# Kernel tuning notes

Hardware: AMD Instinct MI355X
Metric: run time of the kernel (lower is better)

## Reference

```python
import jax, jax.numpy as jnp
import numpy as np

N = 65536   # base nodes
M = 65536   # union local nodes
E = 1048576 # base edges
EL = 1048576 # local edges
K = 131072  # membership entries
F = 128     # in_channels
H = 128     # hidden_dim
L = 2       # num_layers
OUT = 2
ALPHA = 0.9


def setup_inputs() -> dict:
    key = jax.random.key(0)
    ks = jax.random.split(key, 16)
    s = 1.0 / np.sqrt(H)
    return {
        "x": jax.random.normal(ks[0], (N, F), jnp.float32),
        "edge_index": jax.random.randint(ks[1], (2, E), 0, N, jnp.int64 if jax.config.jax_enable_x64 else jnp.int32),
        "edge_weight": jax.random.uniform(ks[2], (E,), jnp.float32),
        "local_x0": jax.random.normal(ks[3], (M, F), jnp.float32),
        "copy2orig": jax.random.randint(ks[4], (M,), 0, N),
        "local_adj_index": jax.random.randint(ks[5], (2, EL), 0, M),
        "local_adj_value": jax.random.uniform(ks[6], (EL,), jnp.float32),
        "memb_idx": jax.random.randint(ks[7], (K,), 0, M),
        "memb_gid": jax.random.randint(ks[8], (K,), 0, 64),
        "B": 64,
        "Wb_in": jax.random.normal(ks[9], (F, H), jnp.float32) * s,
        "bb_in": jnp.zeros((H,), jnp.float32),
        "Wl_in": jax.random.normal(ks[10], (F, H), jnp.float32) * s,
        "bl_in": jnp.zeros((H,), jnp.float32),
        "W_base": jax.random.normal(ks[11], (L, H, H), jnp.float32) * s,
        "b_base": jnp.zeros((L, H), jnp.float32),
        "W_local": jax.random.normal(ks[12], (L, H, H), jnp.float32) * s,
        "b_local": jnp.zeros((L, H), jnp.float32),
        "Wp": jax.random.normal(ks[13], (H, OUT), jnp.float32) * s,
        "bp": jnp.zeros((OUT,), jnp.float32),
    }


def reference(x, edge_index, edge_weight, local_x0, copy2orig, local_adj_index,
              local_adj_value, memb_idx, memb_gid, B, Wb_in, bb_in, Wl_in, bl_in,
              W_base, b_base, W_local, b_local, Wp, bp):
    n = x.shape[0]
    m = local_x0.shape[0]
    # input projections (dropout is identity in eval mode)
    base_x = jax.nn.relu(x @ Wb_in + bb_in)
    local_x = jax.nn.relu(local_x0 @ Wl_in + bl_in)
    src, dst = edge_index[0], edge_index[1]
    lsrc, ldst = local_adj_index[0], local_adj_index[1]
    for l in range(W_base.shape[0]):
        # base graph propagation: normalized-adjacency spmm then linear+relu
        base_agg = jax.ops.segment_sum(base_x[src] * edge_weight[:, None], dst, num_segments=n)
        base_x = jax.nn.relu(base_agg @ W_base[l] + b_base[l])
        # local union-graph propagation + alpha-mix with base features via copy2orig
        local_agg = jax.ops.segment_sum(local_x[lsrc] * local_adj_value[:, None], ldst, num_segments=m)
        mix = ALPHA * local_agg + (1.0 - ALPHA) * base_x[copy2orig]
        local_x = jax.nn.relu(mix @ W_local[l] + b_local[l])
    # scatter-mean pooling by membership (fused sum + count)
    sub = jax.ops.segment_sum(local_x[memb_idx], memb_gid, num_segments=B)
    cnt = jax.ops.segment_sum(jnp.ones((memb_gid.shape[0], 1), local_x.dtype), memb_gid, num_segments=B)
    sub = sub / jnp.maximum(cnt, 1.0)
    return sub @ Wp + bp
```

## Files before the change

kernel.cpp:

```cpp
#include <hip/hip_runtime.h>

typedef __attribute__((ext_vector_type(8))) short bfrag;
typedef __attribute__((ext_vector_type(4))) float ffrag;

__device__ __forceinline__ ushort f2bf(float f) {
    union { float f; unsigned u; } v{f};
    unsigned r = v.u + 0x7fff + ((v.u >> 16) & 1);
    return (ushort)(r >> 16);
}
__device__ __forceinline__ float bf2f(ushort u) {
    union { unsigned u; float f; } v{(unsigned)u << 16};
    return v.f;
}
__device__ __forceinline__ float bflo(unsigned u) {
    union { unsigned u; float f; } v{u << 16};
    return v.f;
}
__device__ __forceinline__ float bfhi(unsigned u) {
    union { unsigned u; float f; } v{u & 0xffff0000u};
    return v.f;
}

#define WDEC (1.f / 65535.f)


__global__ __launch_bounds__(256) void wprep_zero(const float* __restrict__ Wb_in, const float* __restrict__ Wl_in,
                                                  const float* __restrict__ W_base, const float* __restrict__ W_local,
                                                  ushort* __restrict__ out,
                                                  int* __restrict__ z_a, int* __restrict__ z_b,
                                                  int* __restrict__ z_c, int* __restrict__ z_d) {
    const int bid = blockIdx.x;
    const int t = threadIdx.x;
    if (bid < 384) {
        int idx = bid * 256 + t;
        int mat = idx >> 14;
        int i = idx & 16383;
        int nn = i >> 7, kk = i & 127;
        const float* src;
        switch (mat) {
            case 0: src = Wb_in; break;
            case 1: src = Wl_in; break;
            case 2: src = W_base; break;
            case 3: src = W_base + 16384; break;
            case 4: src = W_local; break;
            default: src = W_local + 16384; break;
        }
        out[(size_t)mat * 16384 + i] = f2bf(src[kk * 128 + nn]);
    } else {
        int i = (bid - 384) * 256 + t;
        if (i < 512) { z_a[i] = 0; z_b[i] = 0; }
        if (i < 64) z_c[i] = 0;
        z_d[i] = 0;
    }
}


#define NB 512
#define BSH 7
#define CH2 2048

__global__ __launch_bounds__(256) void hist2p(const int* __restrict__ b_dst, const int* __restrict__ l_dst,
                                              int* __restrict__ b_cnt, int* __restrict__ l_cnt,
                                              const int* __restrict__ memb_gid, int* __restrict__ gcount) {
    __shared__ int h[NB];
    const int bid = blockIdx.x;
    const int t = threadIdx.x;
    if (bid < 512) {
        h[t] = 0;
        h[t + 256] = 0;
        __syncthreads();
        const int g = bid >> 8;
        const int* dst = g ? l_dst : b_dst;
        int* cnt = g ? l_cnt : b_cnt;
        const int base = (bid & 255) * 4096;
#pragma unroll
        for (int u = 0; u < 16; ++u)
            atomicAdd(&h[((unsigned)dst[base + u * 256 + t]) >> BSH], 1);
        __syncthreads();
        atomicAdd(&cnt[t], h[t]);
        atomicAdd(&cnt[t + 256], h[t + 256]);
    } else {
        if (t < 64) h[t] = 0;
        __syncthreads();
        const int base = (bid - 512) * 1024;
#pragma unroll
        for (int u = 0; u < 4; ++u) atomicAdd(&h[memb_gid[base + u * 256 + t]], 1);
        __syncthreads();
        if (t < 64) atomicAdd(&gcount[t], h[t]);
    }
}

__global__ __launch_bounds__(512) void scan2p(const int* __restrict__ b_cnt, int* __restrict__ b_sta, int* __restrict__ b_cur,
                                              const int* __restrict__ l_cnt, int* __restrict__ l_sta, int* __restrict__ l_cur,
                                              const int* __restrict__ gcount, int* __restrict__ gstart,
                                              int* __restrict__ cursor) {
    __shared__ int s[NB];
    const int t = threadIdx.x;
    if (blockIdx.x < 2) {
        const int* cnt = blockIdx.x ? l_cnt : b_cnt;
        int* sta = blockIdx.x ? l_sta : b_sta;
        int* cur = blockIdx.x ? l_cur : b_cur;
        int c = cnt[t];
        s[t] = c;
        __syncthreads();
        for (int o = 1; o < NB; o <<= 1) {
            int add = (t >= o) ? s[t - o] : 0;
            __syncthreads();
            s[t] += add;
            __syncthreads();
        }
        sta[t] = s[t] - c;
        cur[t] = s[t] - c;
        if (t == NB - 1) sta[NB] = s[t];
    } else {
        int c = 0;
        if (t < 64) { c = gcount[t]; s[t] = c; }
        __syncthreads();
        if (t < 64) {
            int acc = 0;
            for (int j = 0; j < t; ++j) acc += s[j];
            gstart[t] = acc;
            cursor[t] = acc;
            if (t == 63) gstart[64] = acc + c;
        }
    }
}

__global__ __launch_bounds__(512) void bucket1b(const int* __restrict__ b_src, const int* __restrict__ b_dst,
                                                const float* __restrict__ b_w, int* __restrict__ b_cur,
                                                int2* __restrict__ b_staged,
                                                const int* __restrict__ l_src, const int* __restrict__ l_dst,
                                                const float* __restrict__ l_w, int* __restrict__ l_cur,
                                                int2* __restrict__ l_staged) {
    __shared__ int cnt_s[NB], base_l[NB], base_g[NB], curs[NB];
    __shared__ int2 stage[CH2];
    __shared__ ushort bb[CH2];
    const int t = threadIdx.x;
    const int g = blockIdx.x >> 9;
    const int* src = g ? l_src : b_src;
    const int* dst = g ? l_dst : b_dst;
    const float* w = g ? l_w : b_w;
    int* bcursor = g ? l_cur : b_cur;
    int2* staged = g ? l_staged : b_staged;
    const int base = (blockIdx.x & 511) * CH2;
    cnt_s[t] = 0;
    __syncthreads();
#pragma unroll
    for (int u = 0; u < CH2 / 512; ++u) {
        int b = ((unsigned)dst[base + u * 512 + t]) >> BSH;
        atomicAdd(&cnt_s[b], 1);
    }
    __syncthreads();
    int v = cnt_s[t];
    base_l[t] = v;
    __syncthreads();
    for (int o = 1; o < NB; o <<= 1) {
        int add = (t >= o) ? base_l[t - o] : 0;
        __syncthreads();
        base_l[t] += add;
        __syncthreads();
    }
    {
        int excl = base_l[t] - v;
        base_l[t] = excl;
        curs[t] = excl;
        base_g[t] = atomicAdd(&bcursor[t], v);
    }
    __syncthreads();
#pragma unroll
    for (int u = 0; u < CH2 / 512; ++u) {
        int e = base + u * 512 + t;
        int d = dst[e];
        int b = ((unsigned)d) >> BSH;
        int p = atomicAdd(&curs[b], 1);
        stage[p] = make_int2((src[e] & 0xffff) | ((d & 127) << 16), __float_as_int(w[e]));
        bb[p] = (ushort)b;
    }
    __syncthreads();
    for (int i = t; i < CH2; i += 512) {
        int b = bb[i];
        staged[base_g[b] + (i - base_l[b])] = stage[i];
    }
}

__global__ __launch_bounds__(512) void bucket2b(const int* __restrict__ b_sta, const int2* __restrict__ b_staged,
                                                int* __restrict__ b_start, int* __restrict__ b_edges,
                                                const int* __restrict__ l_sta, const int2* __restrict__ l_staged,
                                                int* __restrict__ l_start, int* __restrict__ l_edges) {
    __shared__ int cnt[128], excl[128], curs[128];
    const int t = threadIdx.x;
    const int g = blockIdx.x >> 9;
    const int b = blockIdx.x & 511;
    const int* bsta = g ? l_sta : b_sta;
    const int2* staged = g ? l_staged : b_staged;
    int* start = g ? l_start : b_start;
    int* edges = g ? l_edges : b_edges;
    if (t < 128) cnt[t] = 0;
    __syncthreads();
    const int s0 = bsta[b];
    const int s1 = bsta[b + 1];
    for (int i = s0 + t; i < s1; i += 512) {
        int dl = (staged[i].x >> 16) & 127;
        atomicAdd(&cnt[dl], 1);
    }
    __syncthreads();
    int v = 0;
    if (t < 128) { v = cnt[t]; excl[t] = v; }
    __syncthreads();
    for (int o = 1; o < 128; o <<= 1) {
        int add = 0;
        if (t < 128 && t >= o) add = excl[t - o];
        __syncthreads();
        if (t < 128) excl[t] += add;
        __syncthreads();
    }
    if (t < 128) {
        int e = excl[t] - v;
        curs[t] = e;
        start[b * 128 + t] = s0 + e;
        if (b == 511 && t == 127) start[65536] = s1;
    }
    __syncthreads();
    for (int i = s0 + t; i < s1; i += 512) {
        int2 se = staged[i];
        int dl = (se.x >> 16) & 127;
        int p = s0 + atomicAdd(&curs[dl], 1);
        float wv = __int_as_float(se.y);
        unsigned wq = (unsigned)(wv * 65535.f + 0.5f);
        edges[p] = (int)(((unsigned)se.x & 0xffffu) | (wq << 16));
    }
}

#define ASTRIDE 136


__global__ __launch_bounds__(256) void gemm_in2(const float* __restrict__ Ab, const float* __restrict__ Al,
                                                const ushort* __restrict__ Wt,
                                                const float* __restrict__ biasb, const float* __restrict__ biasl,
                                                ushort* __restrict__ Yb, ushort* __restrict__ Yl) {
    __shared__ ushort As[64 * ASTRIDE];
    __shared__ ushort Bs[128 * ASTRIDE];
    const int tid = threadIdx.x;
    const int g = blockIdx.x >> 10;
    const float* A = g ? Al : Ab;
    const ushort* W = Wt + (size_t)g * 16384;
    const float* bias = g ? biasl : biasb;
    ushort* Y = g ? Yl : Yb;
    const int r0 = (blockIdx.x & 1023) * 64;

#pragma unroll
    for (int p = 0; p < 8; ++p) {
        int c = p * 256 + tid;
        int row = c >> 5, o4 = (c & 31) * 4;
        float4 v = *(const float4*)(A + (size_t)(r0 + row) * 128 + o4);
        ushort4 u;
        u.x = f2bf(v.x); u.y = f2bf(v.y); u.z = f2bf(v.z); u.w = f2bf(v.w);
        *(ushort4*)&As[row * ASTRIDE + o4] = u;
    }
#pragma unroll
    for (int p = 0; p < 8; ++p) {
        int c = p * 256 + tid;
        int n = c >> 4, o8 = (c & 15) * 8;
        *(uint4*)&Bs[n * ASTRIDE + o8] = *(const uint4*)(W + n * 128 + o8);
    }
    __syncthreads();

    const int lane = tid & 63;
    const int w = tid >> 6;
    const int wm = (w & 1) * 32;
    const int wn = (w >> 1) * 64;
    const int q = lane >> 4;
    const int l16 = lane & 15;

    ffrag acc[2][4];
#pragma unroll
    for (int mt = 0; mt < 2; ++mt)
#pragma unroll
        for (int nt = 0; nt < 4; ++nt) acc[mt][nt] = (ffrag){0.f, 0.f, 0.f, 0.f};

#pragma unroll
    for (int kc = 0; kc < 4; ++kc) {
        bfrag a[2], b[4];
#pragma unroll
        for (int mt = 0; mt < 2; ++mt)
            a[mt] = *(const bfrag*)&As[(wm + mt * 16 + l16) * ASTRIDE + kc * 32 + q * 8];
#pragma unroll
        for (int nt = 0; nt < 4; ++nt)
            b[nt] = *(const bfrag*)&Bs[(wn + nt * 16 + l16) * ASTRIDE + kc * 32 + q * 8];
#pragma unroll
        for (int mt = 0; mt < 2; ++mt)
#pragma unroll
            for (int nt = 0; nt < 4; ++nt)
                acc[mt][nt] = __builtin_amdgcn_mfma_f32_16x16x32_bf16(a[mt], b[nt], acc[mt][nt], 0, 0, 0);
    }

    float bias_v[4];
#pragma unroll
    for (int nt = 0; nt < 4; ++nt) bias_v[nt] = bias[wn + nt * 16 + l16];
#pragma unroll
    for (int mt = 0; mt < 2; ++mt)
#pragma unroll
        for (int nt = 0; nt < 4; ++nt)
#pragma unroll
            for (int r = 0; r < 4; ++r) {
                int row = r0 + wm + mt * 16 + q * 4 + r;
                int col = wn + nt * 16 + l16;
                float v = fmaxf(acc[mt][nt][r] + bias_v[nt], 0.f);
                Y[(size_t)row * 128 + col] = f2bf(v);
            }
}


template <bool MIX>
__global__ __launch_bounds__(256) void gemm_layer(const ushort* __restrict__ A, const ushort* __restrict__ A2,
                                                  const int* __restrict__ ridx,
                                                  const ushort* __restrict__ Wt, const float* __restrict__ bias,
                                                  ushort* __restrict__ Y) {
    __shared__ ushort As[64 * ASTRIDE];
    __shared__ ushort Bs[128 * ASTRIDE];
    const int tid = threadIdx.x;
    const int r0 = blockIdx.x * 64;

#pragma unroll
    for (int p = 0; p < 4; ++p) {
        int c = p * 256 + tid;
        int row = c >> 4, o8 = (c & 15) * 8;
        uint4 v = *(const uint4*)(A + (size_t)(r0 + row) * 128 + o8);
        if (MIX) {
            int rr = ridx[r0 + row];
            uint4 v2 = *(const uint4*)(A2 + (size_t)rr * 128 + o8);
            uint4 o;
            float x0, x1;
            x0 = 0.9f * bflo(v.x) + 0.1f * bflo(v2.x);
            x1 = 0.9f * bfhi(v.x) + 0.1f * bfhi(v2.x);
            o.x = (unsigned)f2bf(x0) | ((unsigned)f2bf(x1) << 16);
            x0 = 0.9f * bflo(v.y) + 0.1f * bflo(v2.y);
            x1 = 0.9f * bfhi(v.y) + 0.1f * bfhi(v2.y);
            o.y = (unsigned)f2bf(x0) | ((unsigned)f2bf(x1) << 16);
            x0 = 0.9f * bflo(v.z) + 0.1f * bflo(v2.z);
            x1 = 0.9f * bfhi(v.z) + 0.1f * bfhi(v2.z);
            o.z = (unsigned)f2bf(x0) | ((unsigned)f2bf(x1) << 16);
            x0 = 0.9f * bflo(v.w) + 0.1f * bflo(v2.w);
            x1 = 0.9f * bfhi(v.w) + 0.1f * bfhi(v2.w);
            o.w = (unsigned)f2bf(x0) | ((unsigned)f2bf(x1) << 16);
            v = o;
        }
        *(uint4*)&As[row * ASTRIDE + o8] = v;
    }
#pragma unroll
    for (int p = 0; p < 8; ++p) {
        int c = p * 256 + tid;
        int n = c >> 4, o8 = (c & 15) * 8;
        *(uint4*)&Bs[n * ASTRIDE + o8] = *(const uint4*)(Wt + n * 128 + o8);
    }
    __syncthreads();

    const int lane = tid & 63;
    const int w = tid >> 6;
    const int wm = (w & 1) * 32;
    const int wn = (w >> 1) * 64;
    const int q = lane >> 4;
    const int l16 = lane & 15;

    ffrag acc[2][4];
#pragma unroll
    for (int mt = 0; mt < 2; ++mt)
#pragma unroll
        for (int nt = 0; nt < 4; ++nt) acc[mt][nt] = (ffrag){0.f, 0.f, 0.f, 0.f};

#pragma unroll
    for (int kc = 0; kc < 4; ++kc) {
        bfrag a[2], b[4];
#pragma unroll
        for (int mt = 0; mt < 2; ++mt)
            a[mt] = *(const bfrag*)&As[(wm + mt * 16 + l16) * ASTRIDE + kc * 32 + q * 8];
#pragma unroll
        for (int nt = 0; nt < 4; ++nt)
            b[nt] = *(const bfrag*)&Bs[(wn + nt * 16 + l16) * ASTRIDE + kc * 32 + q * 8];
#pragma unroll
        for (int mt = 0; mt < 2; ++mt)
#pragma unroll
            for (int nt = 0; nt < 4; ++nt)
                acc[mt][nt] = __builtin_amdgcn_mfma_f32_16x16x32_bf16(a[mt], b[nt], acc[mt][nt], 0, 0, 0);
    }

    float bias_v[4];
#pragma unroll
    for (int nt = 0; nt < 4; ++nt) bias_v[nt] = bias[wn + nt * 16 + l16];
#pragma unroll
    for (int mt = 0; mt < 2; ++mt)
#pragma unroll
        for (int nt = 0; nt < 4; ++nt)
#pragma unroll
            for (int r = 0; r < 4; ++r) {
                int row = r0 + wm + mt * 16 + q * 4 + r;
                int col = wn + nt * 16 + l16;
                float v = fmaxf(acc[mt][nt][r] + bias_v[nt], 0.f);
                Y[(size_t)row * 128 + col] = f2bf(v);
            }
}


__global__ __launch_bounds__(256) void spmm2(const int* __restrict__ bs_start, const int* __restrict__ bs_edges,
                                             const ushort* __restrict__ Xb, ushort* __restrict__ Yb,
                                             const int* __restrict__ ls_start, const int* __restrict__ ls_edges,
                                             const ushort* __restrict__ Xl, ushort* __restrict__ Yl) {
    const int g = blockIdx.x & 1;
    const int* start = g ? ls_start : bs_start;
    const int* edges = g ? ls_edges : bs_edges;
    const ushort* X = g ? Xl : Xb;
    ushort* Y = g ? Yl : Yb;
    int node = (((blockIdx.x >> 1) * 256) + threadIdx.x) >> 5;
    int lane = threadIdx.x & 31;
    int s0 = start[node];
    int s1 = start[node + 1];
    const int f = lane * 4;
    float a0 = 0.f, a1 = 0.f, a2 = 0.f, a3 = 0.f;
    int e = s0;
    for (; e < s1 && (e & 3); ++e) {
        unsigned pe = (unsigned)edges[e];
        float w = (float)(pe >> 16) * WDEC;
        ushort4 v = *(const ushort4*)(X + ((size_t)(pe & 0xffffu) << 7) + f);
        a0 += w * bf2f(v.x); a1 += w * bf2f(v.y); a2 += w * bf2f(v.z); a3 += w * bf2f(v.w);
    }
    for (; e + 8 <= s1; e += 8) {
        int4 pA = *(const int4*)(edges + e);
        int4 pB = *(const int4*)(edges + e + 4);
        ushort4 v0 = *(const ushort4*)(X + ((size_t)((unsigned)pA.x & 0xffffu) << 7) + f);
        ushort4 v1 = *(const ushort4*)(X + ((size_t)((unsigned)pA.y & 0xffffu) << 7) + f);
        ushort4 v2 = *(const ushort4*)(X + ((size_t)((unsigned)pA.z & 0xffffu) << 7) + f);
        ushort4 v3 = *(const ushort4*)(X + ((size_t)((unsigned)pA.w & 0xffffu) << 7) + f);
        ushort4 v4 = *(const ushort4*)(X + ((size_t)((unsigned)pB.x & 0xffffu) << 7) + f);
        ushort4 v5 = *(const ushort4*)(X + ((size_t)((unsigned)pB.y & 0xffffu) << 7) + f);
        ushort4 v6 = *(const ushort4*)(X + ((size_t)((unsigned)pB.z & 0xffffu) << 7) + f);
        ushort4 v7 = *(const ushort4*)(X + ((size_t)((unsigned)pB.w & 0xffffu) << 7) + f);
        float w0 = (float)((unsigned)pA.x >> 16) * WDEC;
        float w1 = (float)((unsigned)pA.y >> 16) * WDEC;
        float w2 = (float)((unsigned)pA.z >> 16) * WDEC;
        float w3 = (float)((unsigned)pA.w >> 16) * WDEC;
        float w4 = (float)((unsigned)pB.x >> 16) * WDEC;
        float w5 = (float)((unsigned)pB.y >> 16) * WDEC;
        float w6 = (float)((unsigned)pB.z >> 16) * WDEC;
        float w7 = (float)((unsigned)pB.w >> 16) * WDEC;
        a0 += w0 * bf2f(v0.x) + w1 * bf2f(v1.x) + w2 * bf2f(v2.x) + w3 * bf2f(v3.x)
            + w4 * bf2f(v4.x) + w5 * bf2f(v5.x) + w6 * bf2f(v6.x) + w7 * bf2f(v7.x);
        a1 += w0 * bf2f(v0.y) + w1 * bf2f(v1.y) + w2 * bf2f(v2.y) + w3 * bf2f(v3.y)
            + w4 * bf2f(v4.y) + w5 * bf2f(v5.y) + w6 * bf2f(v6.y) + w7 * bf2f(v7.y);
        a2 += w0 * bf2f(v0.z) + w1 * bf2f(v1.z) + w2 * bf2f(v2.z) + w3 * bf2f(v3.z)
            + w4 * bf2f(v4.z) + w5 * bf2f(v5.z) + w6 * bf2f(v6.z) + w7 * bf2f(v7.z);
        a3 += w0 * bf2f(v0.w) + w1 * bf2f(v1.w) + w2 * bf2f(v2.w) + w3 * bf2f(v3.w)
            + w4 * bf2f(v4.w) + w5 * bf2f(v5.w) + w6 * bf2f(v6.w) + w7 * bf2f(v7.w);
    }
    for (; e + 4 <= s1; e += 4) {
        int4 pA = *(const int4*)(edges + e);
        ushort4 v0 = *(const ushort4*)(X + ((size_t)((unsigned)pA.x & 0xffffu) << 7) + f);
        ushort4 v1 = *(const ushort4*)(X + ((size_t)((unsigned)pA.y & 0xffffu) << 7) + f);
        ushort4 v2 = *(const ushort4*)(X + ((size_t)((unsigned)pA.z & 0xffffu) << 7) + f);
        ushort4 v3 = *(const ushort4*)(X + ((size_t)((unsigned)pA.w & 0xffffu) << 7) + f);
        float w0 = (float)((unsigned)pA.x >> 16) * WDEC;
        float w1 = (float)((unsigned)pA.y >> 16) * WDEC;
        float w2 = (float)((unsigned)pA.z >> 16) * WDEC;
        float w3 = (float)((unsigned)pA.w >> 16) * WDEC;
        a0 += w0 * bf2f(v0.x) + w1 * bf2f(v1.x) + w2 * bf2f(v2.x) + w3 * bf2f(v3.x);
        a1 += w0 * bf2f(v0.y) + w1 * bf2f(v1.y) + w2 * bf2f(v2.y) + w3 * bf2f(v3.y);
        a2 += w0 * bf2f(v0.z) + w1 * bf2f(v1.z) + w2 * bf2f(v2.z) + w3 * bf2f(v3.z);
        a3 += w0 * bf2f(v0.w) + w1 * bf2f(v1.w) + w2 * bf2f(v2.w) + w3 * bf2f(v3.w);
    }
    for (; e < s1; ++e) {
        unsigned pe = (unsigned)edges[e];
        float w = (float)(pe >> 16) * WDEC;
        ushort4 v = *(const ushort4*)(X + ((size_t)(pe & 0xffffu) << 7) + f);
        a0 += w * bf2f(v.x); a1 += w * bf2f(v.y); a2 += w * bf2f(v.z); a3 += w * bf2f(v.w);
    }
    ushort4 o;
    o.x = f2bf(a0);
    o.y = f2bf(a1);
    o.z = f2bf(a2);
    o.w = f2bf(a3);
    *(ushort4*)(Y + (size_t)node * 128 + f) = o;
}


__global__ __launch_bounds__(256) void pool_scatter(const int* __restrict__ memb_idx,
                                                    const int* __restrict__ memb_gid,
                                                    int* __restrict__ cursor, int* __restrict__ sorted_idx) {
    __shared__ int lhist[64];
    __shared__ int lbase[64];
    __shared__ int loff[1024];
    int t = threadIdx.x;
    if (t < 64) lhist[t] = 0;
    __syncthreads();
    int base = blockIdx.x * 1024;
    int g[4], ix[4];
#pragma unroll
    for (int u = 0; u < 4; ++u) {
        int e = base + u * 256 + t;
        g[u] = memb_gid[e];
        ix[u] = memb_idx[e];
        loff[u * 256 + t] = atomicAdd(&lhist[g[u]], 1);
    }
    __syncthreads();
    if (t < 64) lbase[t] = atomicAdd(&cursor[t], lhist[t]);
    __syncthreads();
#pragma unroll
    for (int u = 0; u < 4; ++u) {
        int pos = lbase[g[u]] + loff[u * 256 + t];
        sorted_idx[pos] = ix[u];
    }
}

__global__ __launch_bounds__(256) void pool_accum(const int* __restrict__ gstart, const int* __restrict__ sorted_idx,
                                                  const ushort* __restrict__ X, float* __restrict__ gsum) {
    const int g = blockIdx.x >> 5;
    const int sgm = blockIdx.x & 31;
    const int gs = gstart[g];
    const int cnt = gstart[g + 1] - gs;
    const int e_begin = gs + ((cnt * sgm) >> 5);
    const int e_end = gs + ((cnt * (sgm + 1)) >> 5);
    const int t = threadIdx.x;
    const int fp = t & 63;
    const int sub = t >> 6;
    float ax = 0.f, ay = 0.f;
#pragma unroll 4
    for (int e = e_begin + sub; e < e_end; e += 4) {
        int idx = sorted_idx[e];
        ushort2 u = *(const ushort2*)(X + (size_t)idx * 128 + fp * 2);
        ax += bf2f(u.x);
        ay += bf2f(u.y);
    }
    __shared__ float sx[256], sy[256];
    sx[t] = ax;
    sy[t] = ay;
    __syncthreads();
    if (t < 64) {
        atomicAdd(&gsum[g * 128 + fp * 2 + 0], sx[t] + sx[t + 64] + sx[t + 128] + sx[t + 192]);
        atomicAdd(&gsum[g * 128 + fp * 2 + 1], sy[t] + sy[t + 64] + sy[t + 128] + sy[t + 192]);
    }
}


__global__ __launch_bounds__(128) void final_kernel(const float* __restrict__ gsum, const int* __restrict__ gcnt,
                                                    const float* __restrict__ Wp, const float* __restrict__ bp,
                                                    float* __restrict__ out) {
    int t = threadIdx.x;
    int g = t >> 1;
    int o = t & 1;
    float inv = 1.f / fmaxf((float)gcnt[g], 1.f);
    float acc = bp[o];
    for (int f = 0; f < 128; ++f) acc += gsum[g * 128 + f] * inv * Wp[f * 2 + o];
    out[g * 2 + o] = acc;
}


extern "C" void kernel_launch(void* const* d_in, const int* in_sizes, int n_in,
                              void* d_out, int out_size, void* d_ws, size_t ws_size,
                              hipStream_t stream) {
    const float* x              = (const float*)d_in[0];
    const int*   edge_index     = (const int*)d_in[1];
    const float* edge_weight    = (const float*)d_in[2];
    const float* local_x0       = (const float*)d_in[3];
    const int*   copy2orig      = (const int*)d_in[4];
    const int*   local_adj_idx  = (const int*)d_in[5];
    const float* local_adj_val  = (const float*)d_in[6];
    const int*   memb_idx       = (const int*)d_in[7];
    const int*   memb_gid       = (const int*)d_in[8];
    const float* Wb_in          = (const float*)d_in[10];
    const float* bb_in          = (const float*)d_in[11];
    const float* Wl_in          = (const float*)d_in[12];
    const float* bl_in          = (const float*)d_in[13];
    const float* W_base         = (const float*)d_in[14];
    const float* b_base         = (const float*)d_in[15];
    const float* W_local        = (const float*)d_in[16];
    const float* b_local        = (const float*)d_in[17];
    const float* Wp             = (const float*)d_in[18];
    const float* bp             = (const float*)d_in[19];
    float* out = (float*)d_out;

    constexpr int N = 65536, M = 65536, E = 1048576, EL = 1048576, K = 131072, H = 128;

    char* wsb = (char*)d_ws;
    size_t off = 0;
    auto alloc = [&](size_t bytes) -> char* {
        char* p = wsb + off;
        off += (bytes + 255) & ~(size_t)255;
        return p;
    };
    int*    bs_start = (int*)alloc((size_t)(N + 1) * 4);
    int*    bs_edges = (int*)alloc((size_t)E * 4);
    int2*   bs_stage = (int2*)alloc((size_t)E * 8);
    int*    bs_bcnt  = (int*)alloc(NB * 4);
    int*    bs_bsta  = (int*)alloc((NB + 1) * 4);
    int*    bs_bcur  = (int*)alloc(NB * 4);
    int*    ls_start = (int*)alloc((size_t)(M + 1) * 4);
    int*    ls_edges = (int*)alloc((size_t)EL * 4);
    int2*   ls_stage = (int2*)alloc((size_t)EL * 8);
    int*    ls_bcnt  = (int*)alloc(NB * 4);
    int*    ls_bsta  = (int*)alloc((NB + 1) * 4);
    int*    ls_bcur  = (int*)alloc(NB * 4);
    ushort* bufA     = (ushort*)alloc((size_t)N * H * 2);
    ushort* bufB     = (ushort*)alloc((size_t)M * H * 2);
    ushort* bufC     = (ushort*)alloc((size_t)N * H * 2);
    ushort* bufD     = (ushort*)alloc((size_t)M * H * 2);
    ushort* wt       = (ushort*)alloc((size_t)6 * 16384 * 2);
    int*    p_gcnt   = (int*)alloc(64 * 4);
    int*    p_gstart = (int*)alloc(65 * 4);
    int*    p_cursor = (int*)alloc(64 * 4);
    int*    p_sorted = (int*)alloc((size_t)K * 4);
    float*  pool_sum = (float*)alloc(64 * 128 * 4);

    const int* b_src = edge_index;
    const int* b_dst = edge_index + E;
    const int* l_src = local_adj_idx;
    const int* l_dst = local_adj_idx + EL;

    wprep_zero<<<416, 256, 0, stream>>>(Wb_in, Wl_in, W_base, W_local, wt,
                                        bs_bcnt, ls_bcnt, p_gcnt, (int*)pool_sum);

    hist2p<<<640, 256, 0, stream>>>(b_dst, l_dst, bs_bcnt, ls_bcnt, memb_gid, p_gcnt);
    scan2p<<<3, 512, 0, stream>>>(bs_bcnt, bs_bsta, bs_bcur, ls_bcnt, ls_bsta, ls_bcur,
                                  p_gcnt, p_gstart, p_cursor);
    bucket1b<<<1024, 512, 0, stream>>>(b_src, b_dst, edge_weight, bs_bcur, bs_stage,
                                       l_src, l_dst, local_adj_val, ls_bcur, ls_stage);
    bucket2b<<<1024, 512, 0, stream>>>(bs_bsta, bs_stage, bs_start, bs_edges,
                                       ls_bsta, ls_stage, ls_start, ls_edges);

    pool_scatter<<<K / 1024, 256, 0, stream>>>(memb_idx, memb_gid, p_cursor, p_sorted);

    gemm_in2<<<2048, 256, 0, stream>>>(x, local_x0, wt, bb_in, bl_in, bufA, bufB);

    for (int l = 0; l < 2; ++l) {
        spmm2<<<16384, 256, 0, stream>>>(bs_start, bs_edges, bufA, bufC,
                                         ls_start, ls_edges, bufB, bufD);
        gemm_layer<false><<<N / 64, 256, 0, stream>>>(bufC, nullptr, nullptr,
                                                      wt + (size_t)(2 + l) * 16384, b_base + (size_t)l * H, bufA);
        gemm_layer<true><<<M / 64, 256, 0, stream>>>(bufD, bufA, copy2orig,
                                                     wt + (size_t)(4 + l) * 16384, b_local + (size_t)l * H, bufB);
    }

    pool_accum<<<64 * 32, 256, 0, stream>>>(p_gstart, p_sorted, bufB, pool_sum);
    final_kernel<<<1, 128, 0, stream>>>(pool_sum, p_gcnt, Wp, bp, out);
}
```

Baseline: 416.1 us.

## Fuse CSR bucket passes with pool scatter and input GEMM, use wave-shuffle scans

Folds the membership scatter into the first bucketing kernel as extra blocks, and folds the input projection GEMM into the second bucketing kernel as extra blocks. This removes two launches and lets independent work overlap. The prefix scans in scan2p, bucket1 and bucket2 now use wave shuffles plus a per-wave total instead of log-step shared-memory loops with many barriers. The second bucket pass now caches each bucket's edges in LDS and writes the sorted output contiguously, with a global fallback when a bucket exceeds capacity. The trade-off is larger shared memory per block, which lowers occupancy, and mixed block roles inside one launch.

```diff
diff --git a/kernel.cpp b/kernel.cpp
--- a/kernel.cpp
+++ b/kernel.cpp
@@ -58,6 +58,7 @@
 #define NB 512
 #define BSH 7
 #define CH2 2048
+#define SCAP 5632
 
 __global__ __launch_bounds__(256) void hist2p(const int* __restrict__ b_dst, const int* __restrict__ l_dst,
                                               int* __restrict__ b_cnt, int* __restrict__ l_cnt,
@@ -95,23 +96,25 @@
                                               const int* __restrict__ gcount, int* __restrict__ gstart,
                                               int* __restrict__ cursor) {
     __shared__ int s[NB];
+    __shared__ int wtot[8];
     const int t = threadIdx.x;
     if (blockIdx.x < 2) {
         const int* cnt = blockIdx.x ? l_cnt : b_cnt;
         int* sta = blockIdx.x ? l_sta : b_sta;
         int* cur = blockIdx.x ? l_cur : b_cur;
         int c = cnt[t];
-        s[t] = c;
-        __syncthreads();
-        for (int o = 1; o < NB; o <<= 1) {
-            int add = (t >= o) ? s[t - o] : 0;
-            __syncthreads();
-            s[t] += add;
-            __syncthreads();
-        }
-        sta[t] = s[t] - c;
-        cur[t] = s[t] - c;
-        if (t == NB - 1) sta[NB] = s[t];
+        int lane = t & 63, wid = t >> 6;
+        int inc = c;
+        for (int o = 1; o < 64; o <<= 1) { int x = __shfl_up(inc, o); if (lane >= o) inc += x; }
+        if (lane == 63) wtot[wid] = inc;
+        __syncthreads();
+        int wpre = 0;
+#pragma unroll
+        for (int j = 0; j < 8; ++j) if (j < wid) wpre += wtot[j];
+        int excl = wpre + inc - c;
+        sta[t] = excl;
+        cur[t] = excl;
+        if (t == NB - 1) sta[NB] = wpre + inc;
     } else {
         int c = 0;
         if (t < 64) { c = gcount[t]; s[t] = c; }
@@ -126,188 +129,250 @@
     }
 }
 
-__global__ __launch_bounds__(512) void bucket1b(const int* __restrict__ b_src, const int* __restrict__ b_dst,
-                                                const float* __restrict__ b_w, int* __restrict__ b_cur,
-                                                int2* __restrict__ b_staged,
-                                                const int* __restrict__ l_src, const int* __restrict__ l_dst,
-                                                const float* __restrict__ l_w, int* __restrict__ l_cur,
-                                                int2* __restrict__ l_staged) {
+
+__global__ __launch_bounds__(512) void b1p(const int* __restrict__ b_src, const int* __restrict__ b_dst,
+                                           const float* __restrict__ b_w, int* __restrict__ b_cur,
+                                           int2* __restrict__ b_staged,
+                                           const int* __restrict__ l_src, const int* __restrict__ l_dst,
+                                           const float* __restrict__ l_w, int* __restrict__ l_cur,
+                                           int2* __restrict__ l_staged,
+                                           const int* __restrict__ memb_idx, const int* __restrict__ memb_gid,
+                                           int* __restrict__ p_cursor, int* __restrict__ p_sorted) {
     __shared__ int cnt_s[NB], base_l[NB], base_g[NB], curs[NB];
+    __shared__ int wtot[8];
     __shared__ int2 stage[CH2];
     __shared__ ushort bb[CH2];
+    __shared__ int lhist[64], lbase[64], loff[1024];
     const int t = threadIdx.x;
-    const int g = blockIdx.x >> 9;
-    const int* src = g ? l_src : b_src;
-    const int* dst = g ? l_dst : b_dst;
-    const float* w = g ? l_w : b_w;
-    int* bcursor = g ? l_cur : b_cur;
-    int2* staged = g ? l_staged : b_staged;
-    const int base = (blockIdx.x & 511) * CH2;
-    cnt_s[t] = 0;
-    __syncthreads();
-#pragma unroll
-    for (int u = 0; u < CH2 / 512; ++u) {
-        int b = ((unsigned)dst[base + u * 512 + t]) >> BSH;
-        atomicAdd(&cnt_s[b], 1);
-    }
-    __syncthreads();
-    int v = cnt_s[t];
-    base_l[t] = v;
-    __syncthreads();
-    for (int o = 1; o < NB; o <<= 1) {
-        int add = (t >= o) ? base_l[t - o] : 0;
-        __syncthreads();
-        base_l[t] += add;
-        __syncthreads();
-    }
-    {
-        int excl = base_l[t] - v;
+    const int bid = blockIdx.x;
+    if (bid < 1024) {
+        const int g = bid >> 9;
+        const int* src = g ? l_src : b_src;
+        const int* dst = g ? l_dst : b_dst;
+        const float* w = g ? l_w : b_w;
+        int* bcursor = g ? l_cur : b_cur;
+        int2* staged = g ? l_staged : b_staged;
+        const int base = (bid & 511) * CH2;
+        cnt_s[t] = 0;
+        __syncthreads();
+#pragma unroll
+        for (int u = 0; u < CH2 / 512; ++u) {
+            int b = ((unsigned)dst[base + u * 512 + t]) >> BSH;
+            atomicAdd(&cnt_s[b], 1);
+        }
+        __syncthreads();
+        int v = cnt_s[t];
+        int lane = t & 63, wid = t >> 6;
+        int inc = v;
+        for (int o = 1; o < 64; o <<= 1) { int x = __shfl_up(inc, o); if (lane >= o) inc += x; }
+        if (lane == 63) wtot[wid] = inc;
+        __syncthreads();
+        int wpre = 0;
+#pragma unroll
+        for (int j = 0; j < 8; ++j) if (j < wid) wpre += wtot[j];
+        int excl = wpre + inc - v;
         base_l[t] = excl;
         curs[t] = excl;
         base_g[t] = atomicAdd(&bcursor[t], v);
-    }
-    __syncthreads();
-#pragma unroll
-    for (int u = 0; u < CH2 / 512; ++u) {
-        int e = base + u * 512 + t;
-        int d = dst[e];
-        int b = ((unsigned)d) >> BSH;
-        int p = atomicAdd(&curs[b], 1);
-        stage[p] = make_int2((src[e] & 0xffff) | ((d & 127) << 16), __float_as_int(w[e]));
-        bb[p] = (ushort)b;
-    }
-    __syncthreads();
-    for (int i = t; i < CH2; i += 512) {
-        int b = bb[i];
-        staged[base_g[b] + (i - base_l[b])] = stage[i];
-    }
-}
-
-__global__ __launch_bounds__(512) void bucket2b(const int* __restrict__ b_sta, const int2* __restrict__ b_staged,
-                                                int* __restrict__ b_start, int* __restrict__ b_edges,
-                                                const int* __restrict__ l_sta, const int2* __restrict__ l_staged,
-                                                int* __restrict__ l_start, int* __restrict__ l_edges) {
-    __shared__ int cnt[128], excl[128], curs[128];
+        __syncthreads();
+#pragma unroll
+        for (int u = 0; u < CH2 / 512; ++u) {
+            int e = base + u * 512 + t;
+            int d = dst[e];
+            int b = ((unsigned)d) >> BSH;
+            int p = atomicAdd(&curs[b], 1);
+            stage[p] = make_int2((src[e] & 0xffff) | ((d & 127) << 16), __float_as_int(w[e]));
+            bb[p] = (ushort)b;
+        }
+        __syncthreads();
+        for (int i = t; i < CH2; i += 512) {
+            int b = bb[i];
+            staged[base_g[b] + (i - base_l[b])] = stage[i];
+        }
+    } else {
+        if (t < 64) lhist[t] = 0;
+        __syncthreads();
+        const int base = (bid - 1024) * 1024;
+        int g[2], ix[2];
+#pragma unroll
+        for (int u = 0; u < 2; ++u) {
+            int e = base + u * 512 + t;
+            g[u] = memb_gid[e];
+            ix[u] = memb_idx[e];
+            loff[u * 512 + t] = atomicAdd(&lhist[g[u]], 1);
+        }
+        __syncthreads();
+        if (t < 64) lbase[t] = atomicAdd(&p_cursor[t], lhist[t]);
+        __syncthreads();
+#pragma unroll
+        for (int u = 0; u < 2; ++u) {
+            int pos = lbase[g[u]] + loff[u * 512 + t];
+            p_sorted[pos] = ix[u];
+        }
+    }
+}
+
+#define ASTRIDE 136
+
+
+__global__ __launch_bounds__(256) void b2g(const int* __restrict__ b_sta, const int2* __restrict__ b_staged,
+                                           int* __restrict__ b_start, int* __restrict__ b_edges,
+                                           const int* __restrict__ l_sta, const int2* __restrict__ l_staged,
+                                           int* __restrict__ l_start, int* __restrict__ l_edges,
+                                           const float* __restrict__ Ab, const float* __restrict__ Al,
+                                           const ushort* __restrict__ Wt,
+                                           const float* __restrict__ biasb, const float* __restrict__ biasl,
+                                           ushort* __restrict__ Yb, ushort* __restrict__ Yl) {
+    __shared__ __align__(16) char smem[52224];
+    __shared__ int cnt[128], curs[128], wt2[2];
     const int t = threadIdx.x;
-    const int g = blockIdx.x >> 9;
-    const int b = blockIdx.x & 511;
-    const int* bsta = g ? l_sta : b_sta;
-    const int2* staged = g ? l_staged : b_staged;
-    int* start = g ? l_start : b_start;
-    int* edges = g ? l_edges : b_edges;
-    if (t < 128) cnt[t] = 0;
-    __syncthreads();
-    const int s0 = bsta[b];
-    const int s1 = bsta[b + 1];
-    for (int i = s0 + t; i < s1; i += 512) {
-        int dl = (staged[i].x >> 16) & 127;
-        atomicAdd(&cnt[dl], 1);
-    }
-    __syncthreads();
-    int v = 0;
-    if (t < 128) { v = cnt[t]; excl[t] = v; }
-    __syncthreads();
-    for (int o = 1; o < 128; o <<= 1) {
-        int add = 0;
-        if (t < 128 && t >= o) add = excl[t - o];
-        __syncthreads();
-        if (t < 128) excl[t] += add;
-        __syncthreads();
-    }
-    if (t < 128) {
-        int e = excl[t] - v;
-        curs[t] = e;
-        start[b * 128 + t] = s0 + e;
-        if (b == 511 && t == 127) start[65536] = s1;
-    }
-    __syncthreads();
-    for (int i = s0 + t; i < s1; i += 512) {
-        int2 se = staged[i];
-        int dl = (se.x >> 16) & 127;
-        int p = s0 + atomicAdd(&curs[dl], 1);
-        float wv = __int_as_float(se.y);
-        unsigned wq = (unsigned)(wv * 65535.f + 0.5f);
-        edges[p] = (int)(((unsigned)se.x & 0xffffu) | (wq << 16));
-    }
-}
-
-#define ASTRIDE 136
-
-
-__global__ __launch_bounds__(256) void gemm_in2(const float* __restrict__ Ab, const float* __restrict__ Al,
-                                                const ushort* __restrict__ Wt,
-                                                const float* __restrict__ biasb, const float* __restrict__ biasl,
-                                                ushort* __restrict__ Yb, ushort* __restrict__ Yl) {
-    __shared__ ushort As[64 * ASTRIDE];
-    __shared__ ushort Bs[128 * ASTRIDE];
-    const int tid = threadIdx.x;
-    const int g = blockIdx.x >> 10;
-    const float* A = g ? Al : Ab;
-    const ushort* W = Wt + (size_t)g * 16384;
-    const float* bias = g ? biasl : biasb;
-    ushort* Y = g ? Yl : Yb;
-    const int r0 = (blockIdx.x & 1023) * 64;
-
-#pragma unroll
-    for (int p = 0; p < 8; ++p) {
-        int c = p * 256 + tid;
-        int row = c >> 5, o4 = (c & 31) * 4;
-        float4 v = *(const float4*)(A + (size_t)(r0 + row) * 128 + o4);
-        ushort4 u;
-        u.x = f2bf(v.x); u.y = f2bf(v.y); u.z = f2bf(v.z); u.w = f2bf(v.w);
-        *(ushort4*)&As[row * ASTRIDE + o4] = u;
-    }
-#pragma unroll
-    for (int p = 0; p < 8; ++p) {
-        int c = p * 256 + tid;
-        int n = c >> 4, o8 = (c & 15) * 8;
-        *(uint4*)&Bs[n * ASTRIDE + o8] = *(const uint4*)(W + n * 128 + o8);
-    }
-    __syncthreads();
-
-    const int lane = tid & 63;
-    const int w = tid >> 6;
-    const int wm = (w & 1) * 32;
-    const int wn = (w >> 1) * 64;
-    const int q = lane >> 4;
-    const int l16 = lane & 15;
-
-    ffrag acc[2][4];
-#pragma unroll
-    for (int mt = 0; mt < 2; ++mt)
-#pragma unroll
-        for (int nt = 0; nt < 4; ++nt) acc[mt][nt] = (ffrag){0.f, 0.f, 0.f, 0.f};
-
-#pragma unroll
-    for (int kc = 0; kc < 4; ++kc) {
-        bfrag a[2], b[4];
+    const int bid = blockIdx.x;
+    if (bid < 1024) {
+        const int g = bid >> 9;
+        const int b = bid & 511;
+        const int* bsta = g ? l_sta : b_sta;
+        const int2* staged = g ? l_staged : b_staged;
+        int* start = g ? l_start : b_start;
+        int* edges = g ? l_edges : b_edges;
+        const int s0 = bsta[b];
+        const int s1 = bsta[b + 1];
+        const int len = s1 - s0;
+        if (t < 128) cnt[t] = 0;
+        __syncthreads();
+        if (len <= SCAP) {
+            int* seg = (int*)smem;
+            int* ord = (int*)(smem + SCAP * 4);
+            unsigned char* segd = (unsigned char*)(smem + SCAP * 8);
+            for (int i = t; i < len; i += 256) {
+                int2 se = staged[s0 + i];
+                int dl = (se.x >> 16) & 127;
+                unsigned wq = (unsigned)(__int_as_float(se.y) * 65535.f + 0.5f);
+                seg[i] = (int)(((unsigned)se.x & 0xffffu) | (wq << 16));
+                segd[i] = (unsigned char)dl;
+                atomicAdd(&cnt[dl], 1);
+            }
+            __syncthreads();
+            int v = 0, inc = 0;
+            if (t < 128) {
+                v = cnt[t];
+                inc = v;
+                for (int o = 1; o < 64; o <<= 1) { int x = __shfl_up(inc, o); if ((t & 63) >= o) inc += x; }
+                if ((t & 63) == 63) wt2[t >> 6] = inc;
+            }
+            __syncthreads();
+            if (t < 128) {
+                int excl = inc - v + (t >= 64 ? wt2[0] : 0);
+                curs[t] = excl;
+                start[b * 128 + t] = s0 + excl;
+            }
+            if (b == 511 && t == 127) start[65536] = s1;
+            __syncthreads();
+            for (int i = t; i < len; i += 256) {
+                int p = atomicAdd(&curs[segd[i]], 1);
+                ord[p] = seg[i];
+            }
+            __syncthreads();
+            for (int i = t; i < len; i += 256)
+                edges[s0 + i] = ord[i];
+        } else {
+            for (int i = s0 + t; i < s1; i += 256)
+                atomicAdd(&cnt[(staged[i].x >> 16) & 127], 1);
+            __syncthreads();
+            int v = 0, inc = 0;
+            if (t < 128) {
+                v = cnt[t];
+                inc = v;
+                for (int o = 1; o < 64; o <<= 1) { int x = __shfl_up(inc, o); if ((t & 63) >= o) inc += x; }
+                if ((t & 63) == 63) wt2[t >> 6] = inc;
+            }
+            __syncthreads();
+            if (t < 128) {
+                int excl = inc - v + (t >= 64 ? wt2[0] : 0);
+                curs[t] = excl;
+                start[b * 128 + t] = s0 + excl;
+            }
+            if (b == 511 && t == 127) start[65536] = s1;
+            __syncthreads();
+            for (int i = s0 + t; i < s1; i += 256) {
+                int2 se = staged[i];
+                int dl = (se.x >> 16) & 127;
+                unsigned wq = (unsigned)(__int_as_float(se.y) * 65535.f + 0.5f);
+                int p = s0 + atomicAdd(&curs[dl], 1);
+                edges[p] = (int)(((unsigned)se.x & 0xffffu) | (wq << 16));
+            }
+        }
+    } else {
+        ushort* As = (ushort*)smem;
+        ushort* Bs = (ushort*)(smem + 64 * ASTRIDE * 2);
+        const int bid2 = bid - 1024;
+        const int g = bid2 >> 10;
+        const float* A = g ? Al : Ab;
+        const ushort* W = Wt + (size_t)g * 16384;
+        const float* bias = g ? biasl : biasb;
+        ushort* Y = g ? Yl : Yb;
+        const int r0 = (bid2 & 1023) * 64;
+
+#pragma unroll
+        for (int p = 0; p < 8; ++p) {
+            int c = p * 256 + t;
+            int row = c >> 5, o4 = (c & 31) * 4;
+            float4 v = *(const float4*)(A + (size_t)(r0 + row) * 128 + o4);
+            ushort4 u;
+            u.x = f2bf(v.x); u.y = f2bf(v.y); u.z = f2bf(v.z); u.w = f2bf(v.w);
+            *(ushort4*)&As[row * ASTRIDE + o4] = u;
+        }
+#pragma unroll
+        for (int p = 0; p < 8; ++p) {
+            int c = p * 256 + t;
+            int n = c >> 4, o8 = (c & 15) * 8;
+            *(uint4*)&Bs[n * ASTRIDE + o8] = *(const uint4*)(W + n * 128 + o8);
+        }
+        __syncthreads();
+
+        const int lane = t & 63;
+        const int w = t >> 6;
+        const int wm = (w & 1) * 32;
+        const int wn = (w >> 1) * 64;
+        const int q = lane >> 4;
+        const int l16 = lane & 15;
+
+        ffrag acc[2][4];
 #pragma unroll
         for (int mt = 0; mt < 2; ++mt)
-            a[mt] = *(const bfrag*)&As[(wm + mt * 16 + l16) * ASTRIDE + kc * 32 + q * 8];
-#pragma unroll
-        for (int nt = 0; nt < 4; ++nt)
-            b[nt] = *(const bfrag*)&Bs[(wn + nt * 16 + l16) * ASTRIDE + kc * 32 + q * 8];
+#pragma unroll
+            for (int nt = 0; nt < 4; ++nt) acc[mt][nt] = (ffrag){0.f, 0.f, 0.f, 0.f};
+
+#pragma unroll
+        for (int kc = 0; kc < 4; ++kc) {
+            bfrag a[2], b[4];
+#pragma unroll
+            for (int mt = 0; mt < 2; ++mt)
+                a[mt] = *(const bfrag*)&As[(wm + mt * 16 + l16) * ASTRIDE + kc * 32 + q * 8];
+#pragma unroll
+            for (int nt = 0; nt < 4; ++nt)
+                b[nt] = *(const bfrag*)&Bs[(wn + nt * 16 + l16) * ASTRIDE + kc * 32 + q * 8];
+#pragma unroll
+            for (int mt = 0; mt < 2; ++mt)
+#pragma unroll
+                for (int nt = 0; nt < 4; ++nt)
+                    acc[mt][nt] = __builtin_amdgcn_mfma_f32_16x16x32_bf16(a[mt], b[nt], acc[mt][nt], 0, 0, 0);
+        }
+
+        float bias_v[4];
+#pragma unroll
+        for (int nt = 0; nt < 4; ++nt) bias_v[nt] = bias[wn + nt * 16 + l16];
 #pragma unroll
         for (int mt = 0; mt < 2; ++mt)
 #pragma unroll
             for (int nt = 0; nt < 4; ++nt)
-                acc[mt][nt] = __builtin_amdgcn_mfma_f32_16x16x32_bf16(a[mt], b[nt], acc[mt][nt], 0, 0, 0);
-    }
-
-    float bias_v[4];
-#pragma unroll
-    for (int nt = 0; nt < 4; ++nt) bias_v[nt] = bias[wn + nt * 16 + l16];
-#pragma unroll
-    for (int mt = 0; mt < 2; ++mt)
-#pragma unroll
-        for (int nt = 0; nt < 4; ++nt)
-#pragma unroll
-            for (int r = 0; r < 4; ++r) {
-                int row = r0 + wm + mt * 16 + q * 4 + r;
-                int col = wn + nt * 16 + l16;
-                float v = fmaxf(acc[mt][nt][r] + bias_v[nt], 0.f);
-                Y[(size_t)row * 128 + col] = f2bf(v);
-            }
+#pragma unroll
+                for (int r = 0; r < 4; ++r) {
+                    int row = r0 + wm + mt * 16 + q * 4 + r;
+                    int col = wn + nt * 16 + l16;
+                    float v = fmaxf(acc[mt][nt][r] + bias_v[nt], 0.f);
+                    Y[(size_t)row * 128 + col] = f2bf(v);
+                }
+    }
 }
 
 
@@ -480,34 +545,6 @@
     *(ushort4*)(Y + (size_t)node * 128 + f) = o;
 }
 
-
-__global__ __launch_bounds__(256) void pool_scatter(const int* __restrict__ memb_idx,
-                                                    const int* __restrict__ memb_gid,
-                                                    int* __restrict__ cursor, int* __restrict__ sorted_idx) {
-    __shared__ int lhist[64];
-    __shared__ int lbase[64];
-    __shared__ int loff[1024];
-    int t = threadIdx.x;
-    if (t < 64) lhist[t] = 0;
-    __syncthreads();
-    int base = blockIdx.x * 1024;
-    int g[4], ix[4];
-#pragma unroll
-    for (int u = 0; u < 4; ++u) {
-        int e = base + u * 256 + t;
-        g[u] = memb_gid[e];
-        ix[u] = memb_idx[e];
-        loff[u * 256 + t] = atomicAdd(&lhist[g[u]], 1);
-    }
-    __syncthreads();
-    if (t < 64) lbase[t] = atomicAdd(&cursor[t], lhist[t]);
-    __syncthreads();
-#pragma unroll
-    for (int u = 0; u < 4; ++u) {
-        int pos = lbase[g[u]] + loff[u * 256 + t];
-        sorted_idx[pos] = ix[u];
-    }
-}
 
 __global__ __launch_bounds__(256) void pool_accum(const int* __restrict__ gstart, const int* __restrict__ sorted_idx,
                                                   const ushort* __restrict__ X, float* __restrict__ gsum) {
@@ -619,14 +656,14 @@
     hist2p<<<640, 256, 0, stream>>>(b_dst, l_dst, bs_bcnt, ls_bcnt, memb_gid, p_gcnt);
     scan2p<<<3, 512, 0, stream>>>(bs_bcnt, bs_bsta, bs_bcur, ls_bcnt, ls_bsta, ls_bcur,
                                   p_gcnt, p_gstart, p_cursor);
-    bucket1b<<<1024, 512, 0, stream>>>(b_src, b_dst, edge_weight, bs_bcur, bs_stage,
-                                       l_src, l_dst, local_adj_val, ls_bcur, ls_stage);
-    bucket2b<<<1024, 512, 0, stream>>>(bs_bsta, bs_stage, bs_start, bs_edges,
-                                       ls_bsta, ls_stage, ls_start, ls_edges);
-
-    pool_scatter<<<K / 1024, 256, 0, stream>>>(memb_idx, memb_gid, p_cursor, p_sorted);
-
-    gemm_in2<<<2048, 256, 0, stream>>>(x, local_x0, wt, bb_in, bl_in, bufA, bufB);
+
+    b1p<<<1152, 512, 0, stream>>>(b_src, b_dst, edge_weight, bs_bcur, bs_stage,
+                                  l_src, l_dst, local_adj_val, ls_bcur, ls_stage,
+                                  memb_idx, memb_gid, p_cursor, p_sorted);
+
+    b2g<<<3072, 256, 0, stream>>>(bs_bsta, bs_stage, bs_start, bs_edges,
+                                  ls_bsta, ls_stage, ls_start, ls_edges,
+                                  x, local_x0, wt, bb_in, bl_in, bufA, bufB);
 
     for (int l = 0; l < 2; ++l) {
         spmm2<<<16384, 256, 0, stream>>>(bs_start, bs_edges, bufA, bufC,
```

After: 402.1 us. 1.03x faster.
